# Performance work log

Measured on AMD Instinct MI355X. Metric: run time of the kernel, lower is better.

## Reference

```python
import jax, jax.numpy as jnp
import numpy as np

# Module config (matches init_kwargs): inp_modes=[16,4,4,4], out_modes=[16,4,4,4], ranks=[1,8,8,1], 3x3 kernel
C_IN0, C_OUT0 = 16, 16          # leading conv channels
INP_MODES = (4, 4, 4)            # TT input modes -> c_inp = 64
OUT_MODES = (4, 4, 4)            # TT output modes -> c_out = 64
RANKS = (1, 8, 8, 1)
C_INP = int(np.prod(INP_MODES))  # 64
C_OUT = int(np.prod(OUT_MODES))  # 64


def setup_inputs() -> dict:
    key = jax.random.key(0)
    ks = jax.random.split(key, 5)
    x = jax.random.normal(ks[0], (8, C_IN0 * C_INP, 64, 64), jnp.float32)
    kernel = jax.random.normal(ks[1], (C_OUT0, C_IN0, 3, 3), jnp.float32) * (2.0 / (C_IN0 + C_OUT0))
    cores = {}
    for k in range(3):
        m, n = INP_MODES[k], OUT_MODES[k]
        cores[f"core{k}"] = jax.random.normal(ks[2 + k], (RANKS[k], m, n, RANKS[k + 1]), jnp.float32) * (2.0 / (m + n))
    b = jnp.ones((C_OUT,), jnp.float32)
    return {"x": x, "kernel": kernel, **cores, "b": b}


def _tt_matrix(core0, core1, core2):
    # Reconstruct W[(i1 i2 i3), (j1 j2 j3)] from TT cores (r_k, m_k, n_k, r_{k+1}).
    Wm = core0[0]  # (m1, n1, r1)  since r0 == 1
    for c in (core1, core2):
        Wm = jnp.einsum('...r,rmns->...mns', Wm, c)  # append (m_k, n_k) modes
    Wm = Wm[..., 0]  # drop trailing rank (== 1): (m1,n1,m2,n2,m3,n3)
    Wm = jnp.transpose(Wm, (0, 2, 4, 1, 3, 5))       # (m1,m2,m3,n1,n2,n3)
    return Wm.reshape(C_INP, C_OUT)


def reference(x, kernel, core0, core1, core2, b):
    B, Cin, H, W = x.shape  # Cin = C_IN0 * C_INP
    xr = x.reshape(-1, C_IN0, H, W)  # (B*c_inp, c_inp_0, H, W)
    y = jax.lax.conv_general_dilated(
        xr, kernel, window_strides=(1, 1), padding='VALID',
        dimension_numbers=('NCHW', 'OIHW', 'NCHW'))  # (B*c_inp, c_out_0, h, w)
    h, w = y.shape[-2], y.shape[-1]
    # Follow the torch reshape chain exactly
    y = y.reshape(B, C_INP, -1)                 # (B, c_inp, c_out_0*h*w)
    y = jnp.transpose(y, (0, 2, 1)).reshape(-1, C_INP)  # (B*c_out_0*h*w, c_inp)
    Wm = _tt_matrix(core0, core1, core2)        # (c_inp, c_out)
    out = y @ Wm + b                             # (B*c_out_0*h*w, c_out)
    return out.reshape(B, C_OUT0 * C_OUT, h, w)
```

## Files before the change

### kernel.cpp

```cpp
#include <hip/hip_runtime.h>
#include <hip/hip_bf16.h>

#define NB    8
#define NG    64
#define NCI   16
#define NC0   16
#define NJ    64
#define IH    64
#define IW    64
#define OH    62
#define OW    62
#define IPIX  4096
#define OPIX  3844

typedef __attribute__((ext_vector_type(8))) short  short8;
typedef __attribute__((ext_vector_type(4))) short  short4v;
typedef __attribute__((ext_vector_type(4))) float  float4v;

__device__ __forceinline__ unsigned short f2bf(float f) {
    unsigned int u = __builtin_bit_cast(unsigned int, f);
    unsigned int r = (u + 0x7fffu + ((u >> 16) & 1u)) >> 16;
    return (unsigned short)r;
}

__global__ __launch_bounds__(64) void prep_kernel(const float* __restrict__ K,
                                                  const float* __restrict__ c0_,
                                                  const float* __restrict__ c1_,
                                                  const float* __restrict__ c2_,
                                                  unsigned short* __restrict__ wmb,
                                                  unsigned short* __restrict__ kb) {
    int bi = blockIdx.x;
    int l  = threadIdx.x;
    if (bi < 8) {
        int jt = bi >> 1, kh = bi & 1;
        int j = jt * 16 + (l & 15);
        int j1 = j >> 4, j2 = (j >> 2) & 3, j3 = j & 3;
        for (int i = 0; i < 8; ++i) {
            int g = kh * 32 + (l >> 4) * 8 + i;
            int i1 = g >> 4, i2 = (g >> 2) & 3, i3 = g & 3;
            float s = 0.f;
            #pragma unroll
            for (int r1 = 0; r1 < 8; ++r1) {
                float a = c0_[(i1 * 4 + j1) * 8 + r1];
                float t = 0.f;
                #pragma unroll
                for (int r2 = 0; r2 < 8; ++r2) {
                    t += c1_[((r1 * 4 + i2) * 4 + j2) * 8 + r2] *
                         c2_[(r2 * 4 + i3) * 4 + j3];
                }
                s += a * t;
            }
            wmb[(bi * 64 + l) * 8 + i] = f2bf(s);
        }
    } else {
        int c0i = l & 15, q = l >> 4;
        for (int f = 0; f < 5; ++f) {
            int tap = f * 2 + (q >> 1);
            for (int i = 0; i < 8; ++i) {
                int ci = (q & 1) * 8 + i;
                float v = (tap < 9) ? K[(c0i * 16 + ci) * 9 + tap] : 0.f;
                kb[(f * 64 + l) * 8 + i] = f2bf(v);
            }
        }
    }
}

#define PXS  20
#define ROWS 1320

__global__ __launch_bounds__(256, 3) void conv1_kernel(const float* __restrict__ x,
                                                       const unsigned short* __restrict__ kb,
                                                       unsigned short* __restrict__ y) {
    __shared__ unsigned short xl[20 * ROWS];
    int t    = threadIdx.x;
    int bi   = blockIdx.x;
    int band = bi & 3;
    int g    = (bi >> 2) & 63;
    int b    = bi >> 8;
    int y0   = band * 16;

    int lane = t & 63, wv = t >> 6;

    {
        int sub = lane >> 4;
        int px4 = (lane & 15) * 4;
        const float* xg = x + (size_t)(b * 1024 + g * 16) * IPIX;
        #pragma unroll
        for (int i = 0; i < 5; ++i) {
            int grp = i * 4 + wv;
            int cq = grp & 3, rq = grp >> 2;
            int s = rq * 4 + sub;
            int row = y0 + s; if (row > 63) row = 63;
            const float* xr = xg + (size_t)(cq * 4) * IPIX + row * 64 + px4;
            float4v v0 = *(const float4v*)(xr);
            float4v v1 = *(const float4v*)(xr + IPIX);
            float4v v2 = *(const float4v*)(xr + 2 * IPIX);
            float4v v3 = *(const float4v*)(xr + 3 * IPIX);
            unsigned short* dst = xl + s * ROWS + px4 * PXS + cq * 4;
            #pragma unroll
            for (int p = 0; p < 4; ++p) {
                short4v u;
                u[0] = (short)f2bf(v0[p]); u[1] = (short)f2bf(v1[p]);
                u[2] = (short)f2bf(v2[p]); u[3] = (short)f2bf(v3[p]);
                *(short4v*)(dst + p * PXS) = u;
            }
        }
    }
    for (int e = t; e < 20 * 32; e += 256) {
        int s = e >> 5, rem = e & 31;
        xl[s * ROWS + (64 + (rem >> 4)) * PXS + (rem & 15)] = 0;
    }
    __syncthreads();

    int ln = lane & 15, quad = lane >> 4;

    short8 kf[5];
    int off[5];
    #pragma unroll
    for (int f = 0; f < 5; ++f) {
        kf[f] = *(const short8*)(kb + (f * 64 + lane) * 8);
        int tap = f * 2 + (quad >> 1);
        if (tap > 8) tap = 8;
        int dy = tap / 3, dx = tap % 3;
        off[f] = dy * ROWS + dx * PXS;
    }
    int h8 = (quad & 1) * 8;

    for (int k = 0; k < 16; ++k) {
        int tid = wv * 16 + k;
        int yr = tid >> 2, x0 = (tid & 3) * 16;
        int yo = y0 + yr;
        const unsigned short* base = xl + yr * ROWS + (x0 + ln) * PXS + h8;
        float4v acc = {0.f, 0.f, 0.f, 0.f};
        #pragma unroll
        for (int f = 0; f < 5; ++f) {
            const unsigned short* p = base + off[f];
            short4v lo = *(const short4v*)(p);
            short4v hi = *(const short4v*)(p + 4);
            short8 a = __builtin_shufflevector(lo, hi, 0, 1, 2, 3, 4, 5, 6, 7);
            acc = __builtin_amdgcn_mfma_f32_16x16x32_bf16(a, kf[f], acc, 0, 0, 0);
        }
        if (yo < OH) {
            unsigned short* yp = y + ((size_t)(b * 1024 + g * 16 + ln) * 4096
                                      + yo * 64 + x0 + quad * 4);
            short4v o;
            o[0] = (short)f2bf(acc[0]); o[1] = (short)f2bf(acc[1]);
            o[2] = (short)f2bf(acc[2]); o[3] = (short)f2bf(acc[3]);
            *(short4v*)yp = o;
        }
    }
}

__global__ __launch_bounds__(512, 2) void mix3_kernel(const unsigned short* __restrict__ y,
                                                      const unsigned short* __restrict__ wmb,
                                                      const float* __restrict__ bias,
                                                      float* __restrict__ out) {
    __shared__ __align__(16) unsigned short yl[64 * 1024];
    int t    = threadIdx.x;
    int bi   = blockIdx.x;
    int prow = bi % OH;
    int b    = bi / OH;

    {
        int pq = t & 7, grp = t >> 3;
        const unsigned short* yb = y + ((size_t)b * 1024 * 4096) + prow * 64 + pq * 8;
        #pragma unroll
        for (int it = 0; it < 4; ++it) {
            int qd = it * 64 + grp;
            int gq = qd & 15, c0 = qd >> 4;
            const unsigned short* yp = yb + (size_t)(gq * 4 * 16 + c0) * 4096;
            short8 v0 = *(const short8*)(yp);
            short8 v1 = *(const short8*)(yp + 16 * 4096);
            short8 v2 = *(const short8*)(yp + 32 * 4096);
            short8 v3 = *(const short8*)(yp + 48 * 4096);
            int chunk = gq >> 1;
            int gof   = (gq & 1) * 4;
            #pragma unroll
            for (int pp = 0; pp < 8; ++pp) {
                int px = pq * 8 + pp;
                int csw = chunk ^ (c0 & 7) ^ (pq & 7);
                short4v u;
                u[0] = v0[pp]; u[1] = v1[pp]; u[2] = v2[pp]; u[3] = v3[pp];
                *(short4v*)(yl + px * 1024 + c0 * 64 + csw * 8 + gof) = u;
            }
        }
    }
    __syncthreads();

    int lane = t & 63, wv = t >> 6;
    int ln = lane & 15, quad = lane >> 4;

    short8 bf[8];
    #pragma unroll
    for (int q8 = 0; q8 < 8; ++q8)
        bf[q8] = *(const short8*)(wmb + (q8 * 64 + lane) * 8);

    float4v bv[4];
    #pragma unroll
    for (int jt = 0; jt < 4; ++jt)
        bv[jt] = *(const float4v*)(bias + jt * 16 + quad * 4);

    for (int kk = 0; kk < 8; ++kk) {
        int pl = wv * 8 + kk;
        const unsigned short* arow = yl + pl * 1024 + ln * 64;
        int sx = (ln & 7) ^ ((pl >> 3) & 7);
        short8 a0 = *(const short8*)(arow + (((0 + quad) ^ sx) * 8));
        short8 a1 = *(const short8*)(arow + (((4 + quad) ^ sx) * 8));
        if (pl < OW) {
            float* ob = out + (((size_t)(b * 16 + ln) * OPIX) + prow * OW + pl) * NJ
                        + quad * 4;
            #pragma unroll
            for (int jt = 0; jt < 4; ++jt) {
                float4v acc = bv[jt];
                acc = __builtin_amdgcn_mfma_f32_16x16x32_bf16(bf[jt * 2 + 0], a0, acc, 0, 0, 0);
                acc = __builtin_amdgcn_mfma_f32_16x16x32_bf16(bf[jt * 2 + 1], a1, acc, 0, 0, 0);
                *(float4v*)(ob + jt * 16) = acc;
            }
        }
    }
}

__global__ __launch_bounds__(64) void wm_kernel(const float* __restrict__ core0,
                                                const float* __restrict__ core1,
                                                const float* __restrict__ core2,
                                                float* __restrict__ Wm) {
    int g = threadIdx.x;
    int i1 = g >> 4, i2 = (g >> 2) & 3, i3 = g & 3;
    for (int j = 0; j < NJ; ++j) {
        int j1 = j >> 4, j2 = (j >> 2) & 3, j3 = j & 3;
        float s = 0.f;
        #pragma unroll
        for (int r1 = 0; r1 < 8; ++r1) {
            float a = core0[(i1 * 4 + j1) * 8 + r1];
            float t = 0.f;
            #pragma unroll
            for (int r2 = 0; r2 < 8; ++r2) {
                t += core1[((r1 * 4 + i2) * 4 + j2) * 8 + r2] *
                     core2[(r2 * 4 + i3) * 4 + j3];
            }
            s += a * t;
        }
        Wm[g * NJ + j] = s;
    }
}

__global__ __launch_bounds__(256) void fused_fallback(const float* __restrict__ x,
                                                      const float* __restrict__ K,
                                                      const float* __restrict__ Wm,
                                                      const float* __restrict__ bias,
                                                      float* __restrict__ out) {
    __shared__ float wlds[NG * NJ];
    __shared__ float klds[NCI * 9];
    int blk  = blockIdx.x;
    int pblk = blk & 15;
    int c0   = (blk >> 4) & 15;
    int b    = blk >> 8;
    for (int i = threadIdx.x; i < NG * NJ; i += 256) wlds[i] = Wm[i];
    for (int i = threadIdx.x; i < NCI * 9; i += 256) klds[i] = K[c0 * NCI * 9 + i];
    __syncthreads();

    int pix = pblk * 256 + threadIdx.x;
    if (pix >= OPIX) return;
    int yy = pix / OW;
    int xx = pix % OW;

    float acc[NJ];
    #pragma unroll
    for (int j = 0; j < NJ; ++j) acc[j] = 0.f;

    for (int g = 0; g < NG; ++g) {
        float c = 0.f;
        const float* xb = x + ((size_t)(b * NG + g) * NCI) * IPIX;
        for (int ci = 0; ci < NCI; ++ci) {
            #pragma unroll
            for (int dy = 0; dy < 3; ++dy) {
                #pragma unroll
                for (int dx = 0; dx < 3; ++dx) {
                    c += xb[ci * IPIX + (yy + dy) * IW + (xx + dx)] *
                         klds[ci * 9 + dy * 3 + dx];
                }
            }
        }
        const float4* wp = (const float4*)&wlds[g * NJ];
        #pragma unroll
        for (int j4 = 0; j4 < 16; ++j4) {
            float4 w = wp[j4];
            acc[j4 * 4 + 0] += w.x * c;
            acc[j4 * 4 + 1] += w.y * c;
            acc[j4 * 4 + 2] += w.z * c;
            acc[j4 * 4 + 3] += w.w * c;
        }
    }
    #pragma unroll
    for (int j = 0; j < NJ; ++j) {
        out[(((size_t)(b * NC0 + c0) * OPIX) + pix) * NJ + j] = acc[j] + bias[j];
    }
}

extern "C" void kernel_launch(void* const* d_in, const int* in_sizes, int n_in,
                              void* d_out, int out_size, void* d_ws, size_t ws_size,
                              hipStream_t stream) {
    const float* x     = (const float*)d_in[0];
    const float* K     = (const float*)d_in[1];
    const float* core0 = (const float*)d_in[2];
    const float* core1 = (const float*)d_in[3];
    const float* core2 = (const float*)d_in[4];
    const float* bias  = (const float*)d_in[5];
    float* out = (float*)d_out;

    const size_t z_off   = 16384;
    const size_t z_bytes = (size_t)NB * 1024 * 4096 * sizeof(unsigned short);

    if (ws_size >= z_off + z_bytes + 256) {
        unsigned short* wmb = (unsigned short*)d_ws;
        unsigned short* kb  = (unsigned short*)((char*)d_ws + 8192);
        unsigned short* y   = (unsigned short*)((char*)d_ws + z_off);
        prep_kernel<<<9, 64, 0, stream>>>(K, core0, core1, core2, wmb, kb);
        conv1_kernel<<<NB * NG * 4, 256, 0, stream>>>(x, kb, y);
        mix3_kernel<<<NB * OH, 512, 0, stream>>>(y, wmb, bias, out);
    } else {
        float* Wm = (float*)d_ws;
        wm_kernel<<<1, 64, 0, stream>>>(core0, core1, core2, Wm);
        fused_fallback<<<NB * NC0 * 16, 256, 0, stream>>>(x, K, Wm, bias, out);
    }
}
```

Measured before the change: 98.23 us.

## Replace banded conv with rolling-row-buffer kernel that overlaps loads with MFMA

The conv kernel no longer splits each image into four 16-row bands that each reload a 2-row halo. One block now walks all 64 rows of an image group through a 16-slot circular shared-memory row buffer. Each iteration prefetches the next 4 input rows into registers, computes one output row per wave, then writes the prefetched rows into the ring. This removes the halo reloads and overlaps global loads with compute, but it launches 4x fewer blocks, adds a barrier every iteration, and lowers occupancy to 2 blocks per CU.

```diff
diff --git a/kernel.cpp b/kernel.cpp
--- a/kernel.cpp
+++ b/kernel.cpp
@@ -65,89 +65,108 @@
     }
 }
 
-#define PXS  20
-#define ROWS 1320
-
-__global__ __launch_bounds__(256, 3) void conv1_kernel(const float* __restrict__ x,
-                                                       const unsigned short* __restrict__ kb,
-                                                       unsigned short* __restrict__ y) {
-    __shared__ unsigned short xl[20 * ROWS];
-    int t    = threadIdx.x;
-    int bi   = blockIdx.x;
-    int band = bi & 3;
-    int g    = (bi >> 2) & 63;
-    int b    = bi >> 8;
-    int y0   = band * 16;
-
-    int lane = t & 63, wv = t >> 6;
-
-    {
-        int sub = lane >> 4;
-        int px4 = (lane & 15) * 4;
-        const float* xg = x + (size_t)(b * 1024 + g * 16) * IPIX;
-        #pragma unroll
-        for (int i = 0; i < 5; ++i) {
-            int grp = i * 4 + wv;
-            int cq = grp & 3, rq = grp >> 2;
-            int s = rq * 4 + sub;
-            int row = y0 + s; if (row > 63) row = 63;
-            const float* xr = xg + (size_t)(cq * 4) * IPIX + row * 64 + px4;
-            float4v v0 = *(const float4v*)(xr);
-            float4v v1 = *(const float4v*)(xr + IPIX);
-            float4v v2 = *(const float4v*)(xr + 2 * IPIX);
-            float4v v3 = *(const float4v*)(xr + 3 * IPIX);
-            unsigned short* dst = xl + s * ROWS + px4 * PXS + cq * 4;
-            #pragma unroll
-            for (int p = 0; p < 4; ++p) {
-                short4v u;
-                u[0] = (short)f2bf(v0[p]); u[1] = (short)f2bf(v1[p]);
-                u[2] = (short)f2bf(v2[p]); u[3] = (short)f2bf(v3[p]);
-                *(short4v*)(dst + p * PXS) = u;
-            }
-        }
-    }
-    for (int e = t; e < 20 * 32; e += 256) {
-        int s = e >> 5, rem = e & 31;
-        xl[s * ROWS + (64 + (rem >> 4)) * PXS + (rem & 15)] = 0;
-    }
-    __syncthreads();
-
+#define PXS   20
+#define SLOTU 1320
+
+__global__ __launch_bounds__(256, 2) void conv_roll_kernel(const float* __restrict__ x,
+                                                           const unsigned short* __restrict__ kb,
+                                                           unsigned short* __restrict__ y) {
+    __shared__ __align__(16) unsigned short xl[16 * SLOTU];
+    int t = threadIdx.x, lane = t & 63, wv = t >> 6;
+    int g = blockIdx.x & 63, b = blockIdx.x >> 6;
     int ln = lane & 15, quad = lane >> 4;
-
-    short8 kf[5];
-    int off[5];
+    int sub = lane >> 4;
+    int px4 = (lane & 15) * 4;
+
+    const float* xg = x + (size_t)(b * 1024 + g * 16) * IPIX;
+    const float* cbase = xg + (size_t)(wv * 4) * IPIX + sub * 64 + px4;
+
+    short8 kf[5]; int dyf[5], dxo[5];
     #pragma unroll
     for (int f = 0; f < 5; ++f) {
         kf[f] = *(const short8*)(kb + (f * 64 + lane) * 8);
         int tap = f * 2 + (quad >> 1);
         if (tap > 8) tap = 8;
-        int dy = tap / 3, dx = tap % 3;
-        off[f] = dy * ROWS + dx * PXS;
+        dyf[f] = tap / 3;
+        dxo[f] = (tap % 3) * PXS;
     }
     int h8 = (quad & 1) * 8;
 
-    for (int k = 0; k < 16; ++k) {
-        int tid = wv * 16 + k;
-        int yr = tid >> 2, x0 = (tid & 3) * 16;
-        int yo = y0 + yr;
-        const unsigned short* base = xl + yr * ROWS + (x0 + ln) * PXS + h8;
-        float4v acc = {0.f, 0.f, 0.f, 0.f};
+    for (int e = t; e < 512; e += 256) {
+        int s = e >> 5, rem = e & 31;
+        xl[s * SLOTU + (64 + (rem >> 4)) * PXS + (rem & 15)] = 0;
+    }
+
+    #pragma unroll
+    for (int c = 0; c < 2; ++c) {
+        int r0 = c * 4;
+        const float* a = cbase + (size_t)r0 * 64;
+        float4v q0 = *(const float4v*)(a);
+        float4v q1 = *(const float4v*)(a + IPIX);
+        float4v q2 = *(const float4v*)(a + 2 * IPIX);
+        float4v q3 = *(const float4v*)(a + 3 * IPIX);
+        unsigned short* dst = xl + ((r0 + sub) & 15) * SLOTU + px4 * PXS + wv * 4;
         #pragma unroll
-        for (int f = 0; f < 5; ++f) {
-            const unsigned short* p = base + off[f];
-            short4v lo = *(const short4v*)(p);
-            short4v hi = *(const short4v*)(p + 4);
-            short8 a = __builtin_shufflevector(lo, hi, 0, 1, 2, 3, 4, 5, 6, 7);
-            acc = __builtin_amdgcn_mfma_f32_16x16x32_bf16(a, kf[f], acc, 0, 0, 0);
-        }
+        for (int p = 0; p < 4; ++p) {
+            short4v u;
+            u[0] = (short)f2bf(q0[p]); u[1] = (short)f2bf(q1[p]);
+            u[2] = (short)f2bf(q2[p]); u[3] = (short)f2bf(q3[p]);
+            *(short4v*)(dst + p * PXS) = u;
+        }
+    }
+    __syncthreads();
+
+    for (int it = 0; it < 16; ++it) {
+        bool ld = (it <= 13);
+        int r0 = it * 4 + 8;
+        float4v q0, q1, q2, q3;
+        if (ld) {
+            const float* a = cbase + (size_t)r0 * 64;
+            q0 = *(const float4v*)(a);
+            q1 = *(const float4v*)(a + IPIX);
+            q2 = *(const float4v*)(a + 2 * IPIX);
+            q3 = *(const float4v*)(a + 3 * IPIX);
+        }
+
+        int yo = it * 4 + wv;
         if (yo < OH) {
-            unsigned short* yp = y + ((size_t)(b * 1024 + g * 16 + ln) * 4096
-                                      + yo * 64 + x0 + quad * 4);
-            short4v o;
-            o[0] = (short)f2bf(acc[0]); o[1] = (short)f2bf(acc[1]);
-            o[2] = (short)f2bf(acc[2]); o[3] = (short)f2bf(acc[3]);
-            *(short4v*)yp = o;
-        }
+            int sb[5];
+            #pragma unroll
+            for (int f = 0; f < 5; ++f)
+                sb[f] = ((yo + dyf[f]) & 15) * SLOTU;
+            #pragma unroll
+            for (int xt = 0; xt < 4; ++xt) {
+                int x0 = xt * 16;
+                int pxoff = (x0 + ln) * PXS + h8;
+                float4v acc = {0.f, 0.f, 0.f, 0.f};
+                #pragma unroll
+                for (int f = 0; f < 5; ++f) {
+                    const unsigned short* p = xl + sb[f] + pxoff + dxo[f];
+                    short4v lo = *(const short4v*)(p);
+                    short4v hi = *(const short4v*)(p + 4);
+                    short8 a = __builtin_shufflevector(lo, hi, 0, 1, 2, 3, 4, 5, 6, 7);
+                    acc = __builtin_amdgcn_mfma_f32_16x16x32_bf16(a, kf[f], acc, 0, 0, 0);
+                }
+                unsigned short* yp = y + ((size_t)(b * 1024 + g * 16 + ln) * 4096
+                                          + yo * 64 + x0 + quad * 4);
+                short4v o;
+                o[0] = (short)f2bf(acc[0]); o[1] = (short)f2bf(acc[1]);
+                o[2] = (short)f2bf(acc[2]); o[3] = (short)f2bf(acc[3]);
+                *(short4v*)yp = o;
+            }
+        }
+
+        if (ld) {
+            unsigned short* dst = xl + ((r0 + sub) & 15) * SLOTU + px4 * PXS + wv * 4;
+            #pragma unroll
+            for (int p = 0; p < 4; ++p) {
+                short4v u;
+                u[0] = (short)f2bf(q0[p]); u[1] = (short)f2bf(q1[p]);
+                u[2] = (short)f2bf(q2[p]); u[3] = (short)f2bf(q3[p]);
+                *(short4v*)(dst + p * PXS) = u;
+            }
+        }
+        __syncthreads();
     }
 }
 
@@ -316,7 +335,7 @@
         unsigned short* kb  = (unsigned short*)((char*)d_ws + 8192);
         unsigned short* y   = (unsigned short*)((char*)d_ws + z_off);
         prep_kernel<<<9, 64, 0, stream>>>(K, core0, core1, core2, wmb, kb);
-        conv1_kernel<<<NB * NG * 4, 256, 0, stream>>>(x, kb, y);
+        conv_roll_kernel<<<NB * NG, 256, 0, stream>>>(x, kb, y);
         mix3_kernel<<<NB * OH, 512, 0, stream>>>(y, wmb, bias, out);
     } else {
         float* Wm = (float*)d_ws;
```

After: 97.31 us. No clear change (-0.9%).
